# Optimization experiments

Measured on AMD Instinct MI355X. Metric: run time of the kernel, lower is better.

The kernel has to match this reference:

```python
import jax, jax.numpy as jnp
import numpy as np


def setup_inputs() -> dict:
    key = jax.random.key(0)
    ks = jax.random.split(key, 7)
    B, N, H, BIN = 16, 96, 256, 11
    std = 0.1
    return {
        "inputs": jax.random.normal(ks[0], (B, N, H), dtype=jnp.float32),
        "bin_features": jax.random.normal(ks[1], (B, N, N, BIN), dtype=jnp.float32),
        "W_atom": jax.random.normal(ks[2], (H, H), dtype=jnp.float32) * std,
        "W_bin": jax.random.normal(ks[3], (BIN, H), dtype=jnp.float32) * std,
        "b_bin": jnp.zeros((H,), dtype=jnp.float32),
        "w_score": jax.random.normal(ks[4], (H, 1), dtype=jnp.float32) * std,
        "b_score": jnp.zeros((1,), dtype=jnp.float32),
    }


def reference(inputs, bin_features, W_atom, W_bin, b_bin, w_score, b_score):
    # inputs: [B, N, H]; bin_features: [B, N, N, BIN]
    h1 = inputs[:, None, :, :]            # [B, 1, N, H] (atom_hiddens1)
    h2 = inputs[:, :, None, :]            # [B, N, 1, H] (atom_hiddens2)
    atom_pair = h1 + h2                   # [B, N, N, H]
    # Dense(no bias) on pair + Dense(bias) on bin features, then relu
    att_hidden = jax.nn.relu(
        jnp.einsum("bijh,hk->bijk", atom_pair, W_atom)
        + jnp.einsum("bijc,ck->bijk", bin_features, W_bin)
        + b_bin
    )                                      # [B, N, N, H]
    att_score = jax.nn.sigmoid(jnp.einsum("bijk,ko->bijo", att_hidden, w_score) + b_score)  # [B, N, N, 1]
    # att_context = score * atom_hiddens1 (broadcast over i), summed over j (axis 2)
    context = jnp.einsum("bijo,bjh->bih", att_score, inputs)  # [B, N, H]
    return context, atom_pair
```

## Files before the change

kernel.cpp:

```cpp
#include <hip/hip_runtime.h>
#include <math.h>

#define BB 16
#define NN 96
#define HH 256
#define NBIN 11
#define IB 2

typedef float f32x4 __attribute__((ext_vector_type(4)));

template <int CTRL>
__device__ __forceinline__ float dpp_add(float x) {
    int t = __builtin_amdgcn_update_dpp(0, __float_as_int(x),
                                        CTRL, 0xf, 0xf, true);
    return x + __int_as_float(t);
}

__device__ __forceinline__ float wave64_sum_uniform(float x) {
    x = dpp_add<0x111>(x);
    x = dpp_add<0x112>(x);
    x = dpp_add<0x114>(x);
    x = dpp_add<0x118>(x);
    x = dpp_add<0x142>(x);
    x = dpp_add<0x143>(x);
    return __int_as_float(__builtin_amdgcn_readlane(__float_as_int(x), 63));
}

#define ROWS_PER_BLOCK 3

__global__ __launch_bounds__(HH) void proj_kernel(
    const float* __restrict__ inputs,
    const float* __restrict__ W_atom,
    const float* __restrict__ b_bin,
    float* __restrict__ proj)
{
    __shared__ float rows[ROWS_PER_BLOCK][HH];
    const int r0 = blockIdx.x * ROWS_PER_BLOCK;
    const int k  = threadIdx.x;

    #pragma unroll
    for (int r = 0; r < ROWS_PER_BLOCK; ++r)
        rows[r][k] = inputs[(size_t)(r0 + r) * HH + k];
    __syncthreads();

    float acc[ROWS_PER_BLOCK];
    #pragma unroll
    for (int r = 0; r < ROWS_PER_BLOCK; ++r) acc[r] = 0.f;

    #pragma unroll 8
    for (int h = 0; h < HH; ++h) {
        const float w = W_atom[(size_t)h * HH + k];
        #pragma unroll
        for (int r = 0; r < ROWS_PER_BLOCK; ++r)
            acc[r] = fmaf(rows[r][h], w, acc[r]);
    }

    const float halfb = 0.5f * b_bin[k];
    #pragma unroll
    for (int r = 0; r < ROWS_PER_BLOCK; ++r)
        proj[(size_t)(r0 + r) * HH + k] = acc[r] + halfb;
}

__global__ __launch_bounds__(256, 4) void pair_ctx_kernel(
    const float* __restrict__ inputs,
    const float* __restrict__ bin_features,
    const float* __restrict__ W_bin,
    const float* __restrict__ w_score,
    const float* __restrict__ b_score,
    const float* __restrict__ proj,
    float* __restrict__ atom_pair,
    float* __restrict__ context)
{
    const int blk   = blockIdx.x;
    const int b     = blk / (NN / IB);
    const int ip    = blk % (NN / IB);
    const int bi0   = b * NN + IB * ip;
    const int lane  = threadIdx.x & 63;
    const int wave  = threadIdx.x >> 6;
    const int swave = __builtin_amdgcn_readfirstlane(wave);
    const int k4    = lane << 2;

    __shared__ float partial[3][IB * HH];

    const float4 in_i0 = *(const float4*)(inputs + (size_t)bi0 * HH + k4);
    const float4 in_i1 = *(const float4*)(inputs + (size_t)(bi0 + 1) * HH + k4);
    const float4 pr_i0 = *(const float4*)(proj   + (size_t)bi0 * HH + k4);
    const float4 pr_i1 = *(const float4*)(proj   + (size_t)(bi0 + 1) * HH + k4);
    const float4 ws    = *(const float4*)(w_score + k4);
    const float  bsc   = b_score[0];

    float4 wb[NBIN];
    #pragma unroll
    for (int c = 0; c < NBIN; ++c)
        wb[c] = *(const float4*)(W_bin + c * HH + k4);

    const float* inb  = inputs + (size_t)b * NN * HH + k4;
    const float* prb  = proj   + (size_t)b * NN * HH + k4;
    float*       apb0 = atom_pair + (size_t)bi0 * NN * HH + k4;
    float*       apb1 = atom_pair + (size_t)(bi0 + 1) * NN * HH + k4;

    const float* bin0 = bin_features + (size_t)bi0 * NN * NBIN;
    const float* bin1 = bin_features + (size_t)(bi0 + 1) * NN * NBIN;

    float4 acc0 = make_float4(0.f, 0.f, 0.f, 0.f);
    float4 acc1 = make_float4(0.f, 0.f, 0.f, 0.f);

    for (int t = 0; t < 12; ++t) {
        const int j0 = swave + 8 * t;

        float4 inj[2], prj[2];
        #pragma unroll
        for (int u = 0; u < 2; ++u) {
            inj[u] = *(const float4*)(inb + (size_t)(j0 + 4 * u) * HH);
            prj[u] = *(const float4*)(prb + (size_t)(j0 + 4 * u) * HH);
        }

        #pragma unroll
        for (int u = 0; u < 2; ++u) {
            f32x4 ap;
            ap.x = in_i0.x + inj[u].x;  ap.y = in_i0.y + inj[u].y;
            ap.z = in_i0.z + inj[u].z;  ap.w = in_i0.w + inj[u].w;
            __builtin_nontemporal_store(
                ap, (f32x4*)(apb0 + (size_t)(j0 + 4 * u) * HH));
            ap.x = in_i1.x + inj[u].x;  ap.y = in_i1.y + inj[u].y;
            ap.z = in_i1.z + inj[u].z;  ap.w = in_i1.w + inj[u].w;
            __builtin_nontemporal_store(
                ap, (f32x4*)(apb1 + (size_t)(j0 + 4 * u) * HH));
        }

        float part[4];
        #pragma unroll
        for (int u = 0; u < 2; ++u) {
            const int j = j0 + 4 * u;
            #pragma unroll
            for (int ii = 0; ii < 2; ++ii) {
                const float* bp = (ii ? bin1 : bin0) + (size_t)j * NBIN;

                const float4 pri = ii ? pr_i1 : pr_i0;
                float4 v;
                v.x = pri.x + prj[u].x;  v.y = pri.y + prj[u].y;
                v.z = pri.z + prj[u].z;  v.w = pri.w + prj[u].w;
                #pragma unroll
                for (int c = 0; c < NBIN; ++c) {
                    const float bc = bp[c];
                    v.x = fmaf(bc, wb[c].x, v.x);
                    v.y = fmaf(bc, wb[c].y, v.y);
                    v.z = fmaf(bc, wb[c].z, v.z);
                    v.w = fmaf(bc, wb[c].w, v.w);
                }
                v.x = fmaxf(v.x, 0.f); v.y = fmaxf(v.y, 0.f);
                v.z = fmaxf(v.z, 0.f); v.w = fmaxf(v.w, 0.f);
                part[2 * u + ii] =
                    v.x * ws.x + v.y * ws.y + v.z * ws.z + v.w * ws.w;
            }
        }

        float s[4];
        #pragma unroll
        for (int p = 0; p < 4; ++p) {
            const float tot = wave64_sum_uniform(part[p]);
            s[p] = __builtin_amdgcn_rcpf(1.f + __expf(-(tot + bsc)));
        }

        #pragma unroll
        for (int u = 0; u < 2; ++u) {
            acc0.x = fmaf(s[2 * u],     inj[u].x, acc0.x);
            acc0.y = fmaf(s[2 * u],     inj[u].y, acc0.y);
            acc0.z = fmaf(s[2 * u],     inj[u].z, acc0.z);
            acc0.w = fmaf(s[2 * u],     inj[u].w, acc0.w);
            acc1.x = fmaf(s[2 * u + 1], inj[u].x, acc1.x);
            acc1.y = fmaf(s[2 * u + 1], inj[u].y, acc1.y);
            acc1.z = fmaf(s[2 * u + 1], inj[u].z, acc1.z);
            acc1.w = fmaf(s[2 * u + 1], inj[u].w, acc1.w);
        }
    }

    if (wave > 0) {
        *(float4*)(&partial[wave - 1][k4]) = acc0;
        *(float4*)(&partial[wave - 1][HH + k4]) = acc1;
    }
    __syncthreads();
    if (wave == 0) {
        #pragma unroll
        for (int w = 0; w < 3; ++w) {
            const float4 p0 = *(const float4*)(&partial[w][k4]);
            const float4 p1 = *(const float4*)(&partial[w][HH + k4]);
            acc0.x += p0.x; acc0.y += p0.y; acc0.z += p0.z; acc0.w += p0.w;
            acc1.x += p1.x; acc1.y += p1.y; acc1.z += p1.z; acc1.w += p1.w;
        }
        *(float4*)(context + (size_t)bi0 * HH + k4) = acc0;
        *(float4*)(context + (size_t)(bi0 + 1) * HH + k4) = acc1;
    }
}

extern "C" void kernel_launch(void* const* d_in, const int* in_sizes, int n_in,
                              void* d_out, int out_size, void* d_ws, size_t ws_size,
                              hipStream_t stream)
{
    const float* inputs       = (const float*)d_in[0];
    const float* bin_features = (const float*)d_in[1];
    const float* W_atom       = (const float*)d_in[2];
    const float* W_bin        = (const float*)d_in[3];
    const float* b_bin        = (const float*)d_in[4];
    const float* w_score      = (const float*)d_in[5];
    const float* b_score      = (const float*)d_in[6];

    float* context   = (float*)d_out;
    float* atom_pair = (float*)d_out + (size_t)BB * NN * HH;

    float* proj = (float*)d_ws;

    proj_kernel<<<(BB * NN) / ROWS_PER_BLOCK, HH, 0, stream>>>(
        inputs, W_atom, b_bin, proj);

    pair_ctx_kernel<<<(BB * NN) / IB, 256, 0, stream>>>(
        inputs, bin_features, W_bin, w_score, b_score, proj,
        atom_pair, context);
}
```

Before: 48.44 us.

## Split atom_pair writes into a separate kernel from score/context kernel

Moves the atom_pair broadcast-add stores out of the fused pair/context kernel into a dedicated pair_writer kernel with 512-thread blocks, leaving score_ctx_kernel to handle only the score computation and context accumulation. The aim is to let the store-bound write and the compute-bound scoring each run with better-suited occupancy and less register pressure. In exchange it adds an extra launch and rereads the inputs, and the two kernels are serialized on the same stream, so their work can no longer overlap.

New measurement: 68.29 us. 1.41x slower.

```diff
diff --git a/kernel.cpp b/kernel.cpp
--- a/kernel.cpp
+++ b/kernel.cpp
@@ -61,14 +61,46 @@
         proj[(size_t)(r0 + r) * HH + k] = acc[r] + halfb;
 }
 
-__global__ __launch_bounds__(256, 4) void pair_ctx_kernel(
+__global__ __launch_bounds__(512) void pair_writer(
+    const float* __restrict__ inputs,
+    float* __restrict__ atom_pair)
+{
+    const int blk  = blockIdx.x;
+    const int b    = blk / (NN / 2);
+    const int ip   = blk % (NN / 2);
+    const int bi0  = b * NN + 2 * ip;
+    const int lane = threadIdx.x & 63;
+    const int wave = threadIdx.x >> 6;
+    const int k4   = lane << 2;
+
+    const float4 in_i0 = *(const float4*)(inputs + (size_t)bi0 * HH + k4);
+    const float4 in_i1 = *(const float4*)(inputs + (size_t)(bi0 + 1) * HH + k4);
+    const float* inb   = inputs + (size_t)b * NN * HH + k4;
+    float* apb0 = atom_pair + (size_t)bi0 * NN * HH + k4;
+    float* apb1 = atom_pair + (size_t)(bi0 + 1) * NN * HH + k4;
+
+    const int j0 = 12 * wave;
+    #pragma unroll 4
+    for (int t = 0; t < 12; ++t) {
+        const int j = j0 + t;
+        const float4 in_j = *(const float4*)(inb + (size_t)j * HH);
+        f32x4 ap;
+        ap.x = in_i0.x + in_j.x;  ap.y = in_i0.y + in_j.y;
+        ap.z = in_i0.z + in_j.z;  ap.w = in_i0.w + in_j.w;
+        __builtin_nontemporal_store(ap, (f32x4*)(apb0 + (size_t)j * HH));
+        ap.x = in_i1.x + in_j.x;  ap.y = in_i1.y + in_j.y;
+        ap.z = in_i1.z + in_j.z;  ap.w = in_i1.w + in_j.w;
+        __builtin_nontemporal_store(ap, (f32x4*)(apb1 + (size_t)j * HH));
+    }
+}
+
+__global__ __launch_bounds__(256, 4) void score_ctx_kernel(
     const float* __restrict__ inputs,
     const float* __restrict__ bin_features,
     const float* __restrict__ W_bin,
     const float* __restrict__ w_score,
     const float* __restrict__ b_score,
     const float* __restrict__ proj,
-    float* __restrict__ atom_pair,
     float* __restrict__ context)
 {
     const int blk   = blockIdx.x;
@@ -82,10 +114,8 @@
 
     __shared__ float partial[3][IB * HH];
 
-    const float4 in_i0 = *(const float4*)(inputs + (size_t)bi0 * HH + k4);
-    const float4 in_i1 = *(const float4*)(inputs + (size_t)(bi0 + 1) * HH + k4);
-    const float4 pr_i0 = *(const float4*)(proj   + (size_t)bi0 * HH + k4);
-    const float4 pr_i1 = *(const float4*)(proj   + (size_t)(bi0 + 1) * HH + k4);
+    const float4 pr_i0 = *(const float4*)(proj + (size_t)bi0 * HH + k4);
+    const float4 pr_i1 = *(const float4*)(proj + (size_t)(bi0 + 1) * HH + k4);
     const float4 ws    = *(const float4*)(w_score + k4);
     const float  bsc   = b_score[0];
 
@@ -96,8 +126,6 @@
 
     const float* inb  = inputs + (size_t)b * NN * HH + k4;
     const float* prb  = proj   + (size_t)b * NN * HH + k4;
-    float*       apb0 = atom_pair + (size_t)bi0 * NN * HH + k4;
-    float*       apb1 = atom_pair + (size_t)(bi0 + 1) * NN * HH + k4;
 
     const float* bin0 = bin_features + (size_t)bi0 * NN * NBIN;
     const float* bin1 = bin_features + (size_t)(bi0 + 1) * NN * NBIN;
@@ -113,19 +141,6 @@
         for (int u = 0; u < 2; ++u) {
             inj[u] = *(const float4*)(inb + (size_t)(j0 + 4 * u) * HH);
             prj[u] = *(const float4*)(prb + (size_t)(j0 + 4 * u) * HH);
-        }
-
-        #pragma unroll
-        for (int u = 0; u < 2; ++u) {
-            f32x4 ap;
-            ap.x = in_i0.x + inj[u].x;  ap.y = in_i0.y + inj[u].y;
-            ap.z = in_i0.z + inj[u].z;  ap.w = in_i0.w + inj[u].w;
-            __builtin_nontemporal_store(
-                ap, (f32x4*)(apb0 + (size_t)(j0 + 4 * u) * HH));
-            ap.x = in_i1.x + inj[u].x;  ap.y = in_i1.y + inj[u].y;
-            ap.z = in_i1.z + inj[u].z;  ap.w = in_i1.w + inj[u].w;
-            __builtin_nontemporal_store(
-                ap, (f32x4*)(apb1 + (size_t)(j0 + 4 * u) * HH));
         }
 
         float part[4];
@@ -135,7 +150,6 @@
             #pragma unroll
             for (int ii = 0; ii < 2; ++ii) {
                 const float* bp = (ii ? bin1 : bin0) + (size_t)j * NBIN;
-
                 const float4 pri = ii ? pr_i1 : pr_i0;
                 float4 v;
                 v.x = pri.x + prj[u].x;  v.y = pri.y + prj[u].y;
@@ -213,7 +227,8 @@
     proj_kernel<<<(BB * NN) / ROWS_PER_BLOCK, HH, 0, stream>>>(
         inputs, W_atom, b_bin, proj);
 
-    pair_ctx_kernel<<<(BB * NN) / IB, 256, 0, stream>>>(
-        inputs, bin_features, W_bin, w_score, b_score, proj,
-        atom_pair, context);
-}
+    pair_writer<<<(BB * NN) / 2, 512, 0, stream>>>(inputs, atom_pair);
+
+    score_ctx_kernel<<<(BB * NN) / IB, 256, 0, stream>>>(
+        inputs, bin_features, W_bin, w_score, b_score, proj, context);
+}
```
